# Performance work log

Measured on AMD Instinct MI355X. Metric: run time of the kernel, lower is better.

## Reference

```python
import jax, jax.numpy as jnp
import numpy as np

N = 50000          # num nodes
E = 800000         # num edges (avg degree 16)
F_IN = 512         # num_feature
HID = 128          # hid
COM_LAMBDA = 1.0


def setup_inputs() -> dict:
    key = jax.random.key(0)
    k1, k2, k3, k4, k5, k6 = jax.random.split(key, 6)
    v_ori_vals = jax.random.uniform(k1, (E,), dtype=jnp.float32)
    feat = jax.random.normal(k2, (N, F_IN), dtype=jnp.float32)
    v_indices = jax.random.randint(k3, (2, E), 0, N, dtype=jnp.int64)
    # GraphConvolution params
    gcn_w = jax.random.normal(k4, (F_IN, HID), dtype=jnp.float32) / np.sqrt(F_IN)
    gcn_b = jnp.zeros((HID,), dtype=jnp.float32)
    # gen_mlp: Linear(2*hid, 1), xavier_normal init
    std = 1.414 * np.sqrt(2.0 / (2 * HID + 1))
    mlp_w = jax.random.normal(k5, (1, 2 * HID), dtype=jnp.float32) * std
    mlp_b = jnp.zeros((1,), dtype=jnp.float32)
    return {"v_ori_vals": v_ori_vals, "feat": feat, "v_indices": v_indices,
            "num_node": N, "gcn_w": gcn_w, "gcn_b": gcn_b,
            "mlp_w": mlp_w, "mlp_b": mlp_b}


def reference(v_ori_vals, feat, v_indices, num_node, gcn_w, gcn_b, mlp_w, mlp_b):
    row, col = v_indices[0], v_indices[1]
    # gen_gcn: emb = A @ (feat @ W) + b  (SpMM via segment_sum over edges)
    support = feat @ gcn_w                                      # [N, HID]
    emb = jax.ops.segment_sum(v_ori_vals[:, None] * support[col], row,
                              num_segments=num_node) + gcn_b    # [N, HID]
    # gather endpoints, concat, edge-scoring MLP (dropout = identity in eval)
    ff = jnp.concatenate([emb[row], emb[col]], axis=-1)         # [E, 2*HID]
    temp = (ff @ mlp_w.T + mlp_b).reshape(-1)                   # [E]
    # sparse row-wise softmax over columns (dim=1) -> segment softmax by row
    m = jax.ops.segment_max(temp, row, num_segments=num_node)   # [N]
    e = jnp.exp(temp - m[row])                                  # [E]
    s = jax.ops.segment_sum(e, row, num_segments=num_node)      # [N]
    pi = e / s[row]                                             # [E]
    # gen_v = v_ori + com_lambda * pi (values on the shared edge pattern)
    return v_ori_vals + COM_LAMBDA * pi
```

## Files before the change

### kernel.cpp

```cpp
#include <hip/hip_runtime.h>


typedef unsigned int u32;

#define RPB     128
#define CAP     3072
#define NB_MAX  512
#define SB      256
#define GB      782

__global__ void k_prep(const float* __restrict__ W, const float* __restrict__ mw,
                       float* __restrict__ u2, u32* __restrict__ cnt,
                       int F, int H, int nb) {
  if (blockIdx.x == 0)
    for (int s = threadIdx.x; s < nb; s += blockDim.x) cnt[s] = 0;
  int f = blockIdx.x * blockDim.x + threadIdx.x;
  if (f >= F) return;
  const float4* wr = (const float4*)(W + (size_t)f * H);
  const float4* mv = (const float4*)(mw + H);
  float s = 0.f;
  for (int i = 0; i < H / 4; ++i) {
    float4 a = wr[i], b = mv[i];
    s = fmaf(a.x, b.x, fmaf(a.y, b.y, fmaf(a.z, b.z, fmaf(a.w, b.w, s))));
  }
  u2[f] = s;
}

template <int F>
__global__ void __launch_bounds__(1024)
k_fused(const int* __restrict__ row, const int* __restrict__ col,
        const float* __restrict__ v, const float* __restrict__ feat,
        const float* __restrict__ u2, float* __restrict__ q,
        u32* __restrict__ cnt, uint2* __restrict__ rec8,
        int E, int N, int nb) {
  __shared__ u32 h[NB_MAX];
  __shared__ u32 start[NB_MAX];
  const int tid = threadIdx.x;

  if (blockIdx.x < SB) {
    const int chunk = (E + SB - 1) / SB;
    for (int s = tid; s < nb; s += blockDim.x) h[s] = 0;
    __syncthreads();
    const int lo = blockIdx.x * chunk;
    const int hi = min(E, lo + chunk);
    for (int e = lo + tid; e < hi; e += blockDim.x)
      atomicAdd(&h[row[e] >> 7], 1u);
    __syncthreads();
    for (int s = tid; s < nb; s += blockDim.x) {
      u32 c = h[s];
      start[s] = c ? atomicAdd(&cnt[s], c) : 0u;
      h[s] = 0u;
    }
    __syncthreads();
    for (int e = lo + tid; e < hi; e += blockDim.x) {
      int r = row[e];
      int b = r >> 7;
      u32 rank = atomicAdd(&h[b], 1u);
      u32 off  = min(start[b] + rank, (u32)CAP - 1);
      rec8[(size_t)b * CAP + off] =
          make_uint2(((u32)col[e] << 7) | (u32)(r & 127),
                     __float_as_uint(v[e]));
    }
  } else {
    const int lane = tid & 63;
    const float4 ua = *(const float4*)(u2 + lane * 8);
    const float4 ub = *(const float4*)(u2 + lane * 8 + 4);
    const int wid = (blockIdx.x - SB) * (1024 >> 6) + (tid >> 6);
    const int nw  = GB * (1024 >> 6);
    for (int r = wid; r < N; r += nw) {
      const float* fr = feat + (size_t)r * F + lane * 8;
      float4 a = *(const float4*)fr;
      float4 b = *(const float4*)(fr + 4);
      float s = fmaf(a.x, ua.x, fmaf(a.y, ua.y, fmaf(a.z, ua.z,
                fmaf(a.w, ua.w, fmaf(b.x, ub.x, fmaf(b.y, ub.y,
                fmaf(b.z, ub.z, b.w * ub.w)))))));
      s += __shfl_xor(s, 32);
      s += __shfl_xor(s, 16);
      s += __shfl_xor(s, 8);
      s += __shfl_xor(s, 4);
      s += __shfl_xor(s, 2);
      s += __shfl_xor(s, 1);
      if (lane == 0) q[r] = s;
    }
  }
}

__global__ void __launch_bounds__(1024)
k_sum_t(const uint2* __restrict__ rec8, const u32* __restrict__ cnt,
        const float* __restrict__ q, float* __restrict__ t) {
  __shared__ float acc[RPB];
  const int b = blockIdx.x;
  const int tid = threadIdx.x;
  if (tid < RPB) acc[tid] = 0.f;
  __syncthreads();
  const u32 lo = (u32)b * CAP;
  const u32 n  = min(cnt[b], (u32)CAP);
  for (u32 i = tid; i < n; i += blockDim.x) {
    uint2 rr = rec8[lo + i];
    atomicAdd(&acc[rr.x & 127], q[rr.x >> 7] * __uint_as_float(rr.y));
  }
  __syncthreads();
  if (tid < RPB) t[b * RPB + tid] = __expf(acc[tid]);
}

__global__ void __launch_bounds__(1024)
k_sum_invS(const uint2* __restrict__ rec8, const u32* __restrict__ cnt,
           const float* __restrict__ t, float* __restrict__ invS) {
  __shared__ float acc[RPB];
  const int b = blockIdx.x;
  const int tid = threadIdx.x;
  if (tid < RPB) acc[tid] = 0.f;
  __syncthreads();
  const u32 lo = (u32)b * CAP;
  const u32 n  = min(cnt[b], (u32)CAP);
  for (u32 i = tid; i < n; i += blockDim.x) {
    uint2 rr = rec8[lo + i];
    atomicAdd(&acc[rr.x & 127], t[rr.x >> 7]);
  }
  __syncthreads();
  if (tid < RPB) invS[b * RPB + tid] = 1.0f / acc[tid];
}

__global__ void k_out(const int* __restrict__ row, const int* __restrict__ col,
                      const float* __restrict__ vori, const float* __restrict__ t,
                      const float* __restrict__ invS, float* __restrict__ out,
                      int E) {
  int e4 = blockIdx.x * blockDim.x + threadIdx.x;
  int e  = e4 * 4;
  if (e + 3 < E) {
    int4   r4 = *(const int4*)(row + e);
    int4   c4 = *(const int4*)(col + e);
    float4 v4 = *(const float4*)(vori + e);
    float4 o;
    o.x = v4.x + t[c4.x] * invS[r4.x];
    o.y = v4.y + t[c4.y] * invS[r4.y];
    o.z = v4.z + t[c4.z] * invS[r4.z];
    o.w = v4.w + t[c4.w] * invS[r4.w];
    *(float4*)(out + e) = o;
  } else {
    for (; e < E; ++e)
      out[e] = vori[e] + t[col[e]] * invS[row[e]];
  }
}

__global__ void k_gemv_fb(const float* __restrict__ feat, const float* __restrict__ u2,
                          float* __restrict__ q, int N, int F) {
  const int lane = threadIdx.x & 63;
  const int wave = (blockIdx.x * blockDim.x + threadIdx.x) >> 6;
  if (wave >= N) return;
  const float* fr = feat + (size_t)wave * F;
  float a = 0.f;
  for (int i = lane; i < F; i += 64) a = fmaf(fr[i], u2[i], a);
  for (int off = 32; off; off >>= 1) a += __shfl_xor(a, off);
  if (lane == 0) q[wave] = a;
}
__global__ void k_scatter_B_at(const int* __restrict__ row, const int* __restrict__ col,
                               const float* __restrict__ v, const float* __restrict__ q,
                               float* __restrict__ B, int E) {
  int e = blockIdx.x * blockDim.x + threadIdx.x;
  if (e >= E) return;
  atomicAdd(&B[row[e]], v[e] * q[col[e]]);
}
__global__ void k_node_t(const float* __restrict__ B, float* __restrict__ t, int N) {
  int n = blockIdx.x * blockDim.x + threadIdx.x;
  if (n < N) t[n] = __expf(B[n]);
}
__global__ void k_scatter_S_at(const int* __restrict__ row, const int* __restrict__ col,
                               const float* __restrict__ t, float* __restrict__ S, int E) {
  int e = blockIdx.x * blockDim.x + threadIdx.x;
  if (e >= E) return;
  atomicAdd(&S[row[e]], t[col[e]]);
}
__global__ void k_out_div(const int* __restrict__ row, const int* __restrict__ col,
                          const float* __restrict__ vori, const float* __restrict__ t,
                          const float* __restrict__ S, float* __restrict__ out, int E) {
  int e = blockIdx.x * blockDim.x + threadIdx.x;
  if (e >= E) return;
  out[e] = vori[e] + t[col[e]] / S[row[e]];
}

extern "C" void kernel_launch(void* const* d_in, const int* in_sizes, int n_in,
                              void* d_out, int out_size, void* d_ws, size_t ws_size,
                              hipStream_t stream) {
  const float* vori = (const float*)d_in[0];
  const float* feat = (const float*)d_in[1];
  const int*   vind = (const int*)d_in[2];
  const float* W    = (const float*)d_in[4];
  const float* mw   = (const float*)d_in[6];

  const int E = in_sizes[0];
  const int H = in_sizes[6] / 2;
  const int F = in_sizes[4] / H;
  const int N = in_sizes[1] / F;

  const int* row = vind;
  const int* col = vind + E;

  const int nb   = (N + RPB - 1) / RPB;
  const int npad = nb * RPB;

  float* ws   = (float*)d_ws;
  float* u2   = ws;
  float* q    = u2 + F;
  float* t    = q + N;
  float* invS = t + npad;
  u32*   cnt  = (u32*)(invS + npad);
  size_t hdr  = (size_t)((char*)(cnt + nb) - (char*)d_ws);
  hdr = (hdr + 15) & ~(size_t)15;
  uint2* rec8 = (uint2*)((char*)d_ws + hdr);
  size_t need = hdr + (size_t)nb * CAP * sizeof(uint2);

  k_prep<<<(F + 255) / 256, 256, 0, stream>>>(W, mw, u2, cnt, F, H, nb);

  if (ws_size >= need && F == 512 && H % 4 == 0 && nb <= NB_MAX) {
    k_fused<512><<<SB + GB, 1024, 0, stream>>>(row, col, vori, feat, u2, q,
                                               cnt, rec8, E, N, nb);
    k_sum_t<<<nb, 1024, 0, stream>>>(rec8, cnt, q, t);
    k_sum_invS<<<nb, 1024, 0, stream>>>(rec8, cnt, t, invS);
    const int e4 = (E + 3) / 4;
    k_out<<<(e4 + 255) / 256, 256, 0, stream>>>(row, col, vori, t, invS,
                                                (float*)d_out, E);
  } else {
    const int eb  = (E + 255) / 256;
    const int nbk = (N + 255) / 256;
    float* S = invS;
    k_gemv_fb<<<(N * 64 + 255) / 256, 256, 0, stream>>>(feat, u2, q, N, F);
    hipMemsetAsync((void*)S, 0, sizeof(float) * (size_t)npad, stream);
    k_scatter_B_at<<<eb, 256, 0, stream>>>(row, col, vori, q, S, E);
    k_node_t<<<nbk, 256, 0, stream>>>(S, t, N);
    hipMemsetAsync((void*)S, 0, sizeof(float) * (size_t)npad, stream);
    k_scatter_S_at<<<eb, 256, 0, stream>>>(row, col, t, S, E);
    k_out_div<<<eb, 256, 0, stream>>>(row, col, vori, t, S, (float*)d_out, E);
  }
}
```

Before: 207.8 us.

## Merge all stages into one cooperative persistent kernel with grid syncs

Replaces the five separate launches (prep, fused bucket/gemv, two segment reductions, output) with one cooperative kernel sized to the resident block count. Stages are separated by grid.sync instead of kernel boundaries. The goal is to remove launch gaps and tail effects between small kernels. In exchange, each stage runs on a smaller persistent grid (at most two 1024-thread blocks per CU), and grid-wide barriers add their own cost. The bucketing and the feature GEMV now run one after the other inside each block rather than on separate block groups.

```diff
diff --git a/kernel.cpp b/kernel.cpp
--- a/kernel.cpp
+++ b/kernel.cpp
@@ -1,4 +1,7 @@
 #include <hip/hip_runtime.h>
+#include <hip/hip_cooperative_groups.h>
+
+namespace cg = cooperative_groups;
 
 
 typedef unsigned int u32;
@@ -11,9 +14,9 @@
 
 __global__ void k_prep(const float* __restrict__ W, const float* __restrict__ mw,
                        float* __restrict__ u2, u32* __restrict__ cnt,
-                       int F, int H, int nb) {
+                       int F, int H, int nz) {
   if (blockIdx.x == 0)
-    for (int s = threadIdx.x; s < nb; s += blockDim.x) cnt[s] = 0;
+    for (int s = threadIdx.x; s < nz; s += blockDim.x) cnt[s] = 0;
   int f = blockIdx.x * blockDim.x + threadIdx.x;
   if (f >= F) return;
   const float4* wr = (const float4*)(W + (size_t)f * H);
@@ -26,13 +29,156 @@
   u2[f] = s;
 }
 
-template <int F>
+template <int F, int H>
+__global__ void __launch_bounds__(1024)
+k_mega(const int* __restrict__ row, const int* __restrict__ col,
+       const float* __restrict__ vori, const float* __restrict__ feat,
+       const float* __restrict__ W, const float* __restrict__ mw,
+       float* __restrict__ u2, float* __restrict__ q,
+       float* __restrict__ t, float* __restrict__ invS,
+       u32* __restrict__ cnt, uint2* __restrict__ rec8,
+       float* __restrict__ out, int E, int N, int nb) {
+  __shared__ u32 h[NB_MAX];
+  __shared__ u32 start[NB_MAX];
+  __shared__ float acc[RPB];
+  const int tid  = threadIdx.x;
+  const int lane = tid & 63;
+  const int G    = gridDim.x;
+  cg::grid_group grid = cg::this_grid();
+
+  {
+    const int w = blockIdx.x * (1024 >> 6) + (tid >> 6);
+    if (w < F) {
+      float2 a = *(const float2*)(W + (size_t)w * H + lane * 2);
+      float2 b = *(const float2*)(mw + H + lane * 2);
+      float s = fmaf(a.x, b.x, a.y * b.y);
+      s += __shfl_xor(s, 32);
+      s += __shfl_xor(s, 16);
+      s += __shfl_xor(s, 8);
+      s += __shfl_xor(s, 4);
+      s += __shfl_xor(s, 2);
+      s += __shfl_xor(s, 1);
+      if (lane == 0) u2[w] = s;
+    }
+    if (blockIdx.x == G - 1)
+      for (int s2 = tid; s2 < nb; s2 += 1024) cnt[s2] = 0;
+  }
+
+  grid.sync();
+
+  {
+    const int chunk = (E + G - 1) / G;
+    for (int s = tid; s < nb; s += 1024) h[s] = 0;
+    __syncthreads();
+    const int lo = blockIdx.x * chunk;
+    const int hi = min(E, lo + chunk);
+    for (int e = lo + tid; e < hi; e += 1024)
+      atomicAdd(&h[row[e] >> 7], 1u);
+    __syncthreads();
+    for (int s = tid; s < nb; s += 1024) {
+      u32 c = h[s];
+      start[s] = c ? atomicAdd(&cnt[s], c) : 0u;
+      h[s] = 0u;
+    }
+    __syncthreads();
+    for (int e = lo + tid; e < hi; e += 1024) {
+      int r = row[e];
+      int b = r >> 7;
+      u32 rank = atomicAdd(&h[b], 1u);
+      u32 off  = min(start[b] + rank, (u32)(CAP - 1));
+      rec8[(size_t)b * CAP + off] =
+          make_uint2(((u32)col[e] << 7) | (u32)(r & 127),
+                     __float_as_uint(vori[e]));
+    }
+  }
+
+  {
+    const float4 ua = *(const float4*)(u2 + lane * 8);
+    const float4 ub = *(const float4*)(u2 + lane * 8 + 4);
+    const int wid = blockIdx.x * (1024 >> 6) + (tid >> 6);
+    const int nw  = G * (1024 >> 6);
+    for (int r = wid; r < N; r += nw) {
+      const float* fr = feat + (size_t)r * F + lane * 8;
+      float4 a = *(const float4*)fr;
+      float4 b = *(const float4*)(fr + 4);
+      float s = fmaf(a.x, ua.x, fmaf(a.y, ua.y, fmaf(a.z, ua.z,
+                fmaf(a.w, ua.w, fmaf(b.x, ub.x, fmaf(b.y, ub.y,
+                fmaf(b.z, ub.z, b.w * ub.w)))))));
+      s += __shfl_xor(s, 32);
+      s += __shfl_xor(s, 16);
+      s += __shfl_xor(s, 8);
+      s += __shfl_xor(s, 4);
+      s += __shfl_xor(s, 2);
+      s += __shfl_xor(s, 1);
+      if (lane == 0) q[r] = s;
+    }
+  }
+
+  grid.sync();
+
+  for (int b = blockIdx.x; b < nb; b += G) {
+    if (tid < RPB) acc[tid] = 0.f;
+    __syncthreads();
+    const u32 lo = (u32)b * CAP;
+    const u32 n  = min(cnt[b], (u32)CAP);
+    for (u32 i = tid; i < n; i += 1024) {
+      uint2 rr = rec8[lo + i];
+      atomicAdd(&acc[rr.x & 127], q[rr.x >> 7] * __uint_as_float(rr.y));
+    }
+    __syncthreads();
+    if (tid < RPB) t[b * RPB + tid] = __expf(acc[tid]);
+    __syncthreads();
+  }
+
+  grid.sync();
+
+  for (int b = blockIdx.x; b < nb; b += G) {
+    if (tid < RPB) acc[tid] = 0.f;
+    __syncthreads();
+    const u32 lo = (u32)b * CAP;
+    const u32 n  = min(cnt[b], (u32)CAP);
+    for (u32 i = tid; i < n; i += 1024) {
+      uint2 rr = rec8[lo + i];
+      atomicAdd(&acc[rr.x & 127], t[rr.x >> 7]);
+    }
+    __syncthreads();
+    if (tid < RPB) invS[b * RPB + tid] = 1.0f / acc[tid];
+    __syncthreads();
+  }
+
+  grid.sync();
+
+  {
+    const int e4n  = (E + 3) >> 2;
+    const int gtid = blockIdx.x * 1024 + tid;
+    const int step = G * 1024;
+    for (int i = gtid; i < e4n; i += step) {
+      int e = i * 4;
+      if (e + 3 < E) {
+        int4   r4 = *(const int4*)(row + e);
+        int4   c4 = *(const int4*)(col + e);
+        float4 v4 = *(const float4*)(vori + e);
+        float4 o;
+        o.x = v4.x + t[c4.x] * invS[r4.x];
+        o.y = v4.y + t[c4.y] * invS[r4.y];
+        o.z = v4.z + t[c4.z] * invS[r4.z];
+        o.w = v4.w + t[c4.w] * invS[r4.w];
+        *(float4*)(out + e) = o;
+      } else {
+        for (; e < E; ++e)
+          out[e] = vori[e] + t[col[e]] * invS[row[e]];
+      }
+    }
+  }
+}
+
+
 __global__ void __launch_bounds__(1024)
 k_fused(const int* __restrict__ row, const int* __restrict__ col,
         const float* __restrict__ v, const float* __restrict__ feat,
         const float* __restrict__ u2, float* __restrict__ q,
         u32* __restrict__ cnt, uint2* __restrict__ rec8,
-        int E, int N, int nb) {
+        int E, int N, int nb, int F) {
   __shared__ u32 h[NB_MAX];
   __shared__ u32 start[NB_MAX];
   const int tid = threadIdx.x;
@@ -56,7 +202,7 @@
       int r = row[e];
       int b = r >> 7;
       u32 rank = atomicAdd(&h[b], 1u);
-      u32 off  = min(start[b] + rank, (u32)CAP - 1);
+      u32 off  = min(start[b] + rank, (u32)(CAP - 1));
       rec8[(size_t)b * CAP + off] =
           make_uint2(((u32)col[e] << 7) | (u32)(r & 127),
                      __float_as_uint(v[e]));
@@ -68,7 +214,7 @@
     const int wid = (blockIdx.x - SB) * (1024 >> 6) + (tid >> 6);
     const int nw  = GB * (1024 >> 6);
     for (int r = wid; r < N; r += nw) {
-      const float* fr = feat + (size_t)r * F + lane * 8;
+      const float* fr = feat + (size_t)r * 512 + lane * 8;
       float4 a = *(const float4*)fr;
       float4 b = *(const float4*)(fr + 4);
       float s = fmaf(a.x, ua.x, fmaf(a.y, ua.y, fmaf(a.z, ua.z,
@@ -205,31 +351,69 @@
   float* t    = q + N;
   float* invS = t + npad;
   u32*   cnt  = (u32*)(invS + npad);
-  size_t hdr  = (size_t)((char*)(cnt + nb) - (char*)d_ws);
+  size_t hdr  = (size_t)((char*)(cnt + nb + 8) - (char*)d_ws);
   hdr = (hdr + 15) & ~(size_t)15;
   uint2* rec8 = (uint2*)((char*)d_ws + hdr);
   size_t need = hdr + (size_t)nb * CAP * sizeof(uint2);
 
-  k_prep<<<(F + 255) / 256, 256, 0, stream>>>(W, mw, u2, cnt, F, H, nb);
-
-  if (ws_size >= need && F == 512 && H % 4 == 0 && nb <= NB_MAX) {
-    k_fused<512><<<SB + GB, 1024, 0, stream>>>(row, col, vori, feat, u2, q,
-                                               cnt, rec8, E, N, nb);
-    k_sum_t<<<nb, 1024, 0, stream>>>(rec8, cnt, q, t);
-    k_sum_invS<<<nb, 1024, 0, stream>>>(rec8, cnt, t, invS);
-    const int e4 = (E + 3) / 4;
-    k_out<<<(e4 + 255) / 256, 256, 0, stream>>>(row, col, vori, t, invS,
-                                                (float*)d_out, E);
-  } else {
-    const int eb  = (E + 255) / 256;
-    const int nbk = (N + 255) / 256;
-    float* S = invS;
-    k_gemv_fb<<<(N * 64 + 255) / 256, 256, 0, stream>>>(feat, u2, q, N, F);
-    hipMemsetAsync((void*)S, 0, sizeof(float) * (size_t)npad, stream);
-    k_scatter_B_at<<<eb, 256, 0, stream>>>(row, col, vori, q, S, E);
-    k_node_t<<<nbk, 256, 0, stream>>>(S, t, N);
-    hipMemsetAsync((void*)S, 0, sizeof(float) * (size_t)npad, stream);
-    k_scatter_S_at<<<eb, 256, 0, stream>>>(row, col, t, S, E);
-    k_out_div<<<eb, 256, 0, stream>>>(row, col, vori, t, S, (float*)d_out, E);
-  }
-}
+  static int G_cached = -2;
+  if (G_cached == -2) {
+    int dev = 0, coop = 0, cus = 0, bpc = 0;
+    hipGetDevice(&dev);
+    hipError_t ea = hipDeviceGetAttribute(&coop, hipDeviceAttributeCooperativeLaunch, dev);
+    hipError_t eb = hipDeviceGetAttribute(&cus, hipDeviceAttributeMultiprocessorCount, dev);
+    hipError_t ec = hipOccupancyMaxActiveBlocksPerMultiprocessor(&bpc, k_mega<512, 128>, 1024, 0);
+    if (ea == hipSuccess && eb == hipSuccess && ec == hipSuccess &&
+        coop != 0 && bpc > 0 && cus > 0) {
+      if (bpc > 2) bpc = 2;
+      G_cached = bpc * cus;
+    } else {
+      G_cached = 0;
+    }
+  }
+  const int G = G_cached;
+
+  bool done = false;
+  if (G >= 64 && ws_size >= need && F == 512 && H == 128 && nb <= NB_MAX) {
+    float* outp = (float*)d_out;
+    void* kargs[] = {
+      (void*)&row, (void*)&col, (void*)&vori, (void*)&feat,
+      (void*)&W,   (void*)&mw,  (void*)&u2,   (void*)&q,
+      (void*)&t,   (void*)&invS,(void*)&cnt,  (void*)&rec8,
+      (void*)&outp,(void*)&E,   (void*)&N,    (void*)&nb
+    };
+    hipError_t el = hipLaunchCooperativeKernel(
+        reinterpret_cast<const void*>(&k_mega<512, 128>),
+        dim3(G), dim3(1024), kargs, 0, stream);
+    if (el == hipSuccess) {
+      done = true;
+    } else {
+      (void)hipGetLastError();
+      G_cached = 0;
+    }
+  }
+
+  if (!done) {
+    k_prep<<<(F + 255) / 256, 256, 0, stream>>>(W, mw, u2, cnt, F, H, nb + 8);
+    if (ws_size >= need && F == 512 && H % 4 == 0 && nb <= NB_MAX) {
+      k_fused<<<SB + GB, 1024, 0, stream>>>(row, col, vori, feat, u2, q,
+                                            cnt, rec8, E, N, nb, F);
+      k_sum_t<<<nb, 1024, 0, stream>>>(rec8, cnt, q, t);
+      k_sum_invS<<<nb, 1024, 0, stream>>>(rec8, cnt, t, invS);
+      const int e4 = (E + 3) / 4;
+      k_out<<<(e4 + 255) / 256, 256, 0, stream>>>(row, col, vori, t, invS,
+                                                  (float*)d_out, E);
+    } else {
+      const int eb  = (E + 255) / 256;
+      const int nbk = (N + 255) / 256;
+      float* S = invS;
+      k_gemv_fb<<<(N * 64 + 255) / 256, 256, 0, stream>>>(feat, u2, q, N, F);
+      hipMemsetAsync((void*)S, 0, sizeof(float) * (size_t)npad, stream);
+      k_scatter_B_at<<<eb, 256, 0, stream>>>(row, col, vori, q, S, E);
+      k_node_t<<<nbk, 256, 0, stream>>>(S, t, N);
+      hipMemsetAsync((void*)S, 0, sizeof(float) * (size_t)npad, stream);
+      k_scatter_S_at<<<eb, 256, 0, stream>>>(row, col, t, S, E);
+      k_out_div<<<eb, 256, 0, stream>>>(row, col, vori, t, S, (float*)d_out, E);
+    }
+  }
+}
```

New measurement: 326.7 us. 1.57x slower.

## Fuse row-sum and output into per-bucket finish kernel using stored edge ids

Applied to the files above, without the earlier changes.

The bucketing pass now also writes each edge's original index into a parallel recE array. That lets a new k_finish kernel compute the per-row softmax denominator and write the outputs directly, replacing both k_sum_invS and k_out. Every block of the fused kernel now does scatter work followed by the GEMV rows, instead of splitting blocks between the two roles, and the grid shrinks to 512 blocks. The cost is extra workspace for recE, scattered (uncoalesced) output writes, and k_finish handling at most 3072 records per bucket in three register slots.

```diff
diff --git a/kernel.cpp b/kernel.cpp
--- a/kernel.cpp
+++ b/kernel.cpp
@@ -6,14 +6,15 @@
 #define RPB     128
 #define CAP     3072
 #define NB_MAX  512
+#define FG      512
 #define SB      256
 #define GB      782
 
 __global__ void k_prep(const float* __restrict__ W, const float* __restrict__ mw,
                        float* __restrict__ u2, u32* __restrict__ cnt,
-                       int F, int H, int nb) {
+                       int F, int H, int nz) {
   if (blockIdx.x == 0)
-    for (int s = threadIdx.x; s < nb; s += blockDim.x) cnt[s] = 0;
+    for (int s = threadIdx.x; s < nz; s += blockDim.x) cnt[s] = 0;
   int f = blockIdx.x * blockDim.x + threadIdx.x;
   if (f >= F) return;
   const float4* wr = (const float4*)(W + (size_t)f * H);
@@ -28,45 +29,49 @@
 
 template <int F>
 __global__ void __launch_bounds__(1024)
-k_fused(const int* __restrict__ row, const int* __restrict__ col,
-        const float* __restrict__ v, const float* __restrict__ feat,
-        const float* __restrict__ u2, float* __restrict__ q,
-        u32* __restrict__ cnt, uint2* __restrict__ rec8,
-        int E, int N, int nb) {
+k_fused1r(const int* __restrict__ row, const int* __restrict__ col,
+          const float* __restrict__ v, const float* __restrict__ feat,
+          const float* __restrict__ u2, float* __restrict__ q,
+          u32* __restrict__ cnt, uint2* __restrict__ rec8,
+          u32* __restrict__ recE, int E, int N, int nb) {
   __shared__ u32 h[NB_MAX];
   __shared__ u32 start[NB_MAX];
   const int tid = threadIdx.x;
-
-  if (blockIdx.x < SB) {
-    const int chunk = (E + SB - 1) / SB;
-    for (int s = tid; s < nb; s += blockDim.x) h[s] = 0;
+  const int G   = gridDim.x;
+
+  {
+    const int chunk = (E + G - 1) / G;
+    for (int s = tid; s < nb; s += 1024) h[s] = 0;
     __syncthreads();
     const int lo = blockIdx.x * chunk;
     const int hi = min(E, lo + chunk);
-    for (int e = lo + tid; e < hi; e += blockDim.x)
+    for (int e = lo + tid; e < hi; e += 1024)
       atomicAdd(&h[row[e] >> 7], 1u);
     __syncthreads();
-    for (int s = tid; s < nb; s += blockDim.x) {
+    for (int s = tid; s < nb; s += 1024) {
       u32 c = h[s];
       start[s] = c ? atomicAdd(&cnt[s], c) : 0u;
       h[s] = 0u;
     }
     __syncthreads();
-    for (int e = lo + tid; e < hi; e += blockDim.x) {
+    for (int e = lo + tid; e < hi; e += 1024) {
       int r = row[e];
       int b = r >> 7;
       u32 rank = atomicAdd(&h[b], 1u);
-      u32 off  = min(start[b] + rank, (u32)CAP - 1);
-      rec8[(size_t)b * CAP + off] =
-          make_uint2(((u32)col[e] << 7) | (u32)(r & 127),
-                     __float_as_uint(v[e]));
-    }
-  } else {
+      u32 off  = min(start[b] + rank, (u32)(CAP - 1));
+      size_t idx = (size_t)b * CAP + off;
+      rec8[idx] = make_uint2(((u32)col[e] << 7) | (u32)(r & 127),
+                             __float_as_uint(v[e]));
+      recE[idx] = (u32)e;
+    }
+  }
+
+  {
     const int lane = tid & 63;
     const float4 ua = *(const float4*)(u2 + lane * 8);
     const float4 ub = *(const float4*)(u2 + lane * 8 + 4);
-    const int wid = (blockIdx.x - SB) * (1024 >> 6) + (tid >> 6);
-    const int nw  = GB * (1024 >> 6);
+    const int wid = blockIdx.x * (1024 >> 6) + (tid >> 6);
+    const int nw  = G * (1024 >> 6);
     for (int r = wid; r < N; r += nw) {
       const float* fr = feat + (size_t)r * F + lane * 8;
       float4 a = *(const float4*)fr;
@@ -101,6 +106,103 @@
   }
   __syncthreads();
   if (tid < RPB) t[b * RPB + tid] = __expf(acc[tid]);
+}
+
+__global__ void __launch_bounds__(1024)
+k_finish(const uint2* __restrict__ rec8, const u32* __restrict__ recE,
+         const u32* __restrict__ cnt, const float* __restrict__ t,
+         float* __restrict__ out) {
+  __shared__ float acc[RPB];
+  const int b = blockIdx.x;
+  const int tid = threadIdx.x;
+  if (tid < RPB) acc[tid] = 0.f;
+  __syncthreads();
+  const u32 lo = (u32)b * CAP;
+  const u32 n  = min(cnt[b], (u32)CAP);
+  bool  ok[3];
+  u32   cr[3], ee[3];
+  float vv[3], tc[3];
+#pragma unroll
+  for (int k = 0; k < 3; ++k) {
+    u32 i = (u32)tid + (u32)k * 1024u;
+    ok[k] = (i < n);
+    cr[k] = 0; ee[k] = 0; vv[k] = 0.f; tc[k] = 0.f;
+    if (ok[k]) {
+      uint2 rr = rec8[lo + i];
+      cr[k] = rr.x;
+      vv[k] = __uint_as_float(rr.y);
+      ee[k] = recE[lo + i];
+      float tv = t[rr.x >> 7];
+      tc[k] = tv;
+      atomicAdd(&acc[rr.x & 127], tv);
+    }
+  }
+  __syncthreads();
+  if (tid < RPB) acc[tid] = 1.0f / acc[tid];
+  __syncthreads();
+#pragma unroll
+  for (int k = 0; k < 3; ++k)
+    if (ok[k])
+      out[ee[k]] = vv[k] + tc[k] * acc[cr[k] & 127];
+}
+
+
+__global__ void __launch_bounds__(1024)
+k_fused(const int* __restrict__ row, const int* __restrict__ col,
+        const float* __restrict__ v, const float* __restrict__ feat,
+        const float* __restrict__ u2, float* __restrict__ q,
+        u32* __restrict__ cnt, uint2* __restrict__ rec8,
+        int E, int N, int nb, int F) {
+  __shared__ u32 h[NB_MAX];
+  __shared__ u32 start[NB_MAX];
+  const int tid = threadIdx.x;
+
+  if (blockIdx.x < SB) {
+    const int chunk = (E + SB - 1) / SB;
+    for (int s = tid; s < nb; s += blockDim.x) h[s] = 0;
+    __syncthreads();
+    const int lo = blockIdx.x * chunk;
+    const int hi = min(E, lo + chunk);
+    for (int e = lo + tid; e < hi; e += blockDim.x)
+      atomicAdd(&h[row[e] >> 7], 1u);
+    __syncthreads();
+    for (int s = tid; s < nb; s += blockDim.x) {
+      u32 c = h[s];
+      start[s] = c ? atomicAdd(&cnt[s], c) : 0u;
+      h[s] = 0u;
+    }
+    __syncthreads();
+    for (int e = lo + tid; e < hi; e += blockDim.x) {
+      int r = row[e];
+      int b = r >> 7;
+      u32 rank = atomicAdd(&h[b], 1u);
+      u32 off  = min(start[b] + rank, (u32)(CAP - 1));
+      rec8[(size_t)b * CAP + off] =
+          make_uint2(((u32)col[e] << 7) | (u32)(r & 127),
+                     __float_as_uint(v[e]));
+    }
+  } else {
+    const int lane = tid & 63;
+    const float4 ua = *(const float4*)(u2 + lane * 8);
+    const float4 ub = *(const float4*)(u2 + lane * 8 + 4);
+    const int wid = (blockIdx.x - SB) * (1024 >> 6) + (tid >> 6);
+    const int nw  = GB * (1024 >> 6);
+    for (int r = wid; r < N; r += nw) {
+      const float* fr = feat + (size_t)r * 512 + lane * 8;
+      float4 a = *(const float4*)fr;
+      float4 b = *(const float4*)(fr + 4);
+      float s = fmaf(a.x, ua.x, fmaf(a.y, ua.y, fmaf(a.z, ua.z,
+                fmaf(a.w, ua.w, fmaf(b.x, ub.x, fmaf(b.y, ub.y,
+                fmaf(b.z, ub.z, b.w * ub.w)))))));
+      s += __shfl_xor(s, 32);
+      s += __shfl_xor(s, 16);
+      s += __shfl_xor(s, 8);
+      s += __shfl_xor(s, 4);
+      s += __shfl_xor(s, 2);
+      s += __shfl_xor(s, 1);
+      if (lane == 0) q[r] = s;
+    }
+  }
 }
 
 __global__ void __launch_bounds__(1024)
@@ -205,16 +307,23 @@
   float* t    = q + N;
   float* invS = t + npad;
   u32*   cnt  = (u32*)(invS + npad);
-  size_t hdr  = (size_t)((char*)(cnt + nb) - (char*)d_ws);
+  size_t hdr  = (size_t)((char*)(cnt + nb + 8) - (char*)d_ws);
   hdr = (hdr + 15) & ~(size_t)15;
   uint2* rec8 = (uint2*)((char*)d_ws + hdr);
-  size_t need = hdr + (size_t)nb * CAP * sizeof(uint2);
-
-  k_prep<<<(F + 255) / 256, 256, 0, stream>>>(W, mw, u2, cnt, F, H, nb);
+  u32*   recE = (u32*)(rec8 + (size_t)nb * CAP);
+  size_t need = hdr + (size_t)nb * CAP * (sizeof(uint2) + sizeof(u32));
+  size_t need9 = hdr + (size_t)nb * CAP * sizeof(uint2);
+
+  k_prep<<<(F + 255) / 256, 256, 0, stream>>>(W, mw, u2, cnt, F, H, nb + 8);
 
   if (ws_size >= need && F == 512 && H % 4 == 0 && nb <= NB_MAX) {
-    k_fused<512><<<SB + GB, 1024, 0, stream>>>(row, col, vori, feat, u2, q,
-                                               cnt, rec8, E, N, nb);
+    k_fused1r<512><<<FG, 1024, 0, stream>>>(row, col, vori, feat, u2, q,
+                                            cnt, rec8, recE, E, N, nb);
+    k_sum_t<<<nb, 1024, 0, stream>>>(rec8, cnt, q, t);
+    k_finish<<<nb, 1024, 0, stream>>>(rec8, recE, cnt, t, (float*)d_out);
+  } else if (ws_size >= need9 && F == 512 && H % 4 == 0 && nb <= NB_MAX) {
+    k_fused<<<SB + GB, 1024, 0, stream>>>(row, col, vori, feat, u2, q,
+                                          cnt, rec8, E, N, nb, F);
     k_sum_t<<<nb, 1024, 0, stream>>>(rec8, cnt, q, t);
     k_sum_invS<<<nb, 1024, 0, stream>>>(rec8, cnt, t, invS);
     const int e4 = (E + 3) / 4;
```

New measurement: 216.5 us. +4.2%, slower.

## Fuse normalization and output into bucketed pass using stored edge indices

Applied to the files above, without the earlier changes.

During bucketing, the original edge index of each record is now stored in a new recE array. A new k_finish kernel uses it to compute the row sums, their reciprocals and the final output in one block pass, writing results back to the original edge positions. This replaces the separate invS kernel and the edge-order output kernel, which re-read row, col and v_ori and gathered t and invS. Per-bucket counters are also padded to 64 bytes so global atomics on neighbouring buckets do not share a cache line. The cost is an extra 4-byte write and read per edge and scattered output stores. The fallback path still passes recE to k_fused even though its workspace check does not reserve space for it, so that path can write out of bounds.

```diff
diff --git a/kernel.cpp b/kernel.cpp
--- a/kernel.cpp
+++ b/kernel.cpp
@@ -6,14 +6,15 @@
 #define RPB     128
 #define CAP     3072
 #define NB_MAX  512
+#define CPAD    16
 #define SB      256
 #define GB      782
 
 __global__ void k_prep(const float* __restrict__ W, const float* __restrict__ mw,
                        float* __restrict__ u2, u32* __restrict__ cnt,
-                       int F, int H, int nb) {
+                       int F, int H, int nz) {
   if (blockIdx.x == 0)
-    for (int s = threadIdx.x; s < nb; s += blockDim.x) cnt[s] = 0;
+    for (int s = threadIdx.x; s < nz; s += blockDim.x) cnt[s] = 0;
   int f = blockIdx.x * blockDim.x + threadIdx.x;
   if (f >= F) return;
   const float4* wr = (const float4*)(W + (size_t)f * H);
@@ -32,7 +33,7 @@
         const float* __restrict__ v, const float* __restrict__ feat,
         const float* __restrict__ u2, float* __restrict__ q,
         u32* __restrict__ cnt, uint2* __restrict__ rec8,
-        int E, int N, int nb) {
+        u32* __restrict__ recE, int E, int N, int nb) {
   __shared__ u32 h[NB_MAX];
   __shared__ u32 start[NB_MAX];
   const int tid = threadIdx.x;
@@ -48,7 +49,7 @@
     __syncthreads();
     for (int s = tid; s < nb; s += blockDim.x) {
       u32 c = h[s];
-      start[s] = c ? atomicAdd(&cnt[s], c) : 0u;
+      start[s] = c ? atomicAdd(&cnt[(size_t)s * CPAD], c) : 0u;
       h[s] = 0u;
     }
     __syncthreads();
@@ -56,10 +57,11 @@
       int r = row[e];
       int b = r >> 7;
       u32 rank = atomicAdd(&h[b], 1u);
-      u32 off  = min(start[b] + rank, (u32)CAP - 1);
-      rec8[(size_t)b * CAP + off] =
-          make_uint2(((u32)col[e] << 7) | (u32)(r & 127),
-                     __float_as_uint(v[e]));
+      u32 off  = min(start[b] + rank, (u32)(CAP - 1));
+      size_t idx = (size_t)b * CAP + off;
+      rec8[idx] = make_uint2(((u32)col[e] << 7) | (u32)(r & 127),
+                             __float_as_uint(v[e]));
+      recE[idx] = (u32)e;
     }
   } else {
     const int lane = tid & 63;
@@ -94,7 +96,7 @@
   if (tid < RPB) acc[tid] = 0.f;
   __syncthreads();
   const u32 lo = (u32)b * CAP;
-  const u32 n  = min(cnt[b], (u32)CAP);
+  const u32 n  = min(cnt[(size_t)b * CPAD], (u32)CAP);
   for (u32 i = tid; i < n; i += blockDim.x) {
     uint2 rr = rec8[lo + i];
     atomicAdd(&acc[rr.x & 127], q[rr.x >> 7] * __uint_as_float(rr.y));
@@ -102,6 +104,45 @@
   __syncthreads();
   if (tid < RPB) t[b * RPB + tid] = __expf(acc[tid]);
 }
+
+__global__ void __launch_bounds__(1024)
+k_finish(const uint2* __restrict__ rec8, const u32* __restrict__ recE,
+         const u32* __restrict__ cnt, const float* __restrict__ t,
+         float* __restrict__ out) {
+  __shared__ float acc[RPB];
+  const int b = blockIdx.x;
+  const int tid = threadIdx.x;
+  if (tid < RPB) acc[tid] = 0.f;
+  __syncthreads();
+  const u32 lo = (u32)b * CAP;
+  const u32 n  = min(cnt[(size_t)b * CPAD], (u32)CAP);
+  bool  ok[3];
+  u32   cr[3], ee[3];
+  float vv[3], tc[3];
+#pragma unroll
+  for (int k = 0; k < 3; ++k) {
+    u32 i = (u32)tid + (u32)k * 1024u;
+    ok[k] = (i < n);
+    cr[k] = 0; ee[k] = 0; vv[k] = 0.f; tc[k] = 0.f;
+    if (ok[k]) {
+      uint2 rr = rec8[lo + i];
+      cr[k] = rr.x;
+      vv[k] = __uint_as_float(rr.y);
+      ee[k] = recE[lo + i];
+      float tv = t[rr.x >> 7];
+      tc[k] = tv;
+      atomicAdd(&acc[rr.x & 127], tv);
+    }
+  }
+  __syncthreads();
+  if (tid < RPB) acc[tid] = 1.0f / acc[tid];
+  __syncthreads();
+#pragma unroll
+  for (int k = 0; k < 3; ++k)
+    if (ok[k])
+      out[ee[k]] = vv[k] + tc[k] * acc[cr[k] & 127];
+}
+
 
 __global__ void __launch_bounds__(1024)
 k_sum_invS(const uint2* __restrict__ rec8, const u32* __restrict__ cnt,
@@ -112,7 +153,7 @@
   if (tid < RPB) acc[tid] = 0.f;
   __syncthreads();
   const u32 lo = (u32)b * CAP;
-  const u32 n  = min(cnt[b], (u32)CAP);
+  const u32 n  = min(cnt[(size_t)b * CPAD], (u32)CAP);
   for (u32 i = tid; i < n; i += blockDim.x) {
     uint2 rr = rec8[lo + i];
     atomicAdd(&acc[rr.x & 127], t[rr.x >> 7]);
@@ -205,16 +246,23 @@
   float* t    = q + N;
   float* invS = t + npad;
   u32*   cnt  = (u32*)(invS + npad);
-  size_t hdr  = (size_t)((char*)(cnt + nb) - (char*)d_ws);
-  hdr = (hdr + 15) & ~(size_t)15;
+  size_t hdr  = (size_t)((char*)(cnt + (size_t)nb * CPAD + 16) - (char*)d_ws);
+  hdr = (hdr + 63) & ~(size_t)63;
   uint2* rec8 = (uint2*)((char*)d_ws + hdr);
-  size_t need = hdr + (size_t)nb * CAP * sizeof(uint2);
-
-  k_prep<<<(F + 255) / 256, 256, 0, stream>>>(W, mw, u2, cnt, F, H, nb);
+  u32*   recE = (u32*)(rec8 + (size_t)nb * CAP);
+  size_t need  = hdr + (size_t)nb * CAP * (sizeof(uint2) + sizeof(u32));
+  size_t need9 = hdr + (size_t)nb * CAP * sizeof(uint2);
+
+  k_prep<<<(F + 255) / 256, 256, 0, stream>>>(W, mw, u2, cnt, F, H, nb * CPAD);
 
   if (ws_size >= need && F == 512 && H % 4 == 0 && nb <= NB_MAX) {
     k_fused<512><<<SB + GB, 1024, 0, stream>>>(row, col, vori, feat, u2, q,
-                                               cnt, rec8, E, N, nb);
+                                               cnt, rec8, recE, E, N, nb);
+    k_sum_t<<<nb, 1024, 0, stream>>>(rec8, cnt, q, t);
+    k_finish<<<nb, 1024, 0, stream>>>(rec8, recE, cnt, t, (float*)d_out);
+  } else if (ws_size >= need9 && F == 512 && H % 4 == 0 && nb <= NB_MAX) {
+    k_fused<512><<<SB + GB, 1024, 0, stream>>>(row, col, vori, feat, u2, q,
+                                               cnt, rec8, recE, E, N, nb);
     k_sum_t<<<nb, 1024, 0, stream>>>(rec8, cnt, q, t);
     k_sum_invS<<<nb, 1024, 0, stream>>>(rec8, cnt, t, invS);
     const int e4 = (E + 3) / 4;
```

Result: slower. 214.7 us (+3.3%).
